# Kernel optimization log

Hardware: AMD Instinct MI355X
Metric: run time of the kernel (lower is better)

## Reference

```python
import jax, jax.numpy as jnp
import numpy as np

B, Z, A = 1024, 512, 8          # batch_size, z_dim, action_dim
AH, ZH = 64, 512                # action_hidden_dim, z_hidden_dim
N_NEG = 100                     # n_neg_actions
TEMP = 0.1                      # temperature
TOP_K = (1, 3, 10)


def forward_model(z, a, Wa, ba, W1, b1, W2, b2):
    # MLP forward model with skip connection (z_delta=True):
    # embed action, concat with z, 2-layer MLP predicting a delta.
    h_a = jax.nn.relu(a @ Wa + ba)                                   # [..., AH]
    h = jax.nn.relu(jnp.concatenate([jnp.broadcast_to(z, a.shape[:-1] + (Z,)), h_a], axis=-1) @ W1 + b1)  # [..., ZH]
    delta = h @ W2 + b2                                              # [..., Z]
    return z + delta


def setup_inputs() -> dict:
    key = jax.random.key(0)
    ks = jax.random.split(key, 8)
    def w(k, shape, fan_in):
        return jax.random.normal(k, shape, jnp.float32) / np.float32(np.sqrt(fan_in))
    z = jax.random.normal(ks[0], (B, Z), jnp.float32)
    z_next = jax.random.normal(ks[1], (B, Z), jnp.float32)
    z_next_hat = jax.random.normal(ks[2], (B, Z), jnp.float32)
    actions = jax.random.normal(ks[3], (B, A), jnp.float32)
    Wa = w(ks[4], (A, AH), A)
    ba = jnp.zeros((AH,), jnp.float32)
    W1 = w(ks[5], (Z + AH, ZH), Z + AH)
    b1 = jnp.zeros((ZH,), jnp.float32)
    W2 = w(ks[6], (ZH, Z), ZH)
    b2 = jnp.zeros((Z,), jnp.float32)
    return {"z": z, "z_next": z_next, "z_next_hat": z_next_hat, "actions": actions,
            "Wa": Wa, "ba": ba, "W1": W1, "b1": b1, "W2": W2, "b2": b2}


def reference(z, z_next, z_next_hat, actions, Wa, ba, W1, b1, W2, b2):
    # ControlCPC.compute_loss with dot_product_similarity, vectorized:
    # the Python loop over n_neg_actions rolled-action forward-model calls
    # becomes one batched [n-1, B, ...] forward-model evaluation.
    batch = z.shape[0]
    n = min(N_NEG, batch)
    sim = z_next @ z_next_hat.T                                      # [B, B] positives on diagonal
    shifts = jnp.arange(1, n)
    neg_actions = jax.vmap(lambda i: jnp.roll(actions, -i, axis=0))(shifts)  # [n-1, B, A]
    z_hat_neg = forward_model(z[None], neg_actions, Wa, ba, W1, b1, W2, b2)  # [n-1, B, Z]
    neg_sim = jnp.einsum('nbz,bz->bn', z_hat_neg, z_next)            # diag of similarity per shift
    sim_mat = jnp.concatenate([sim, neg_sim], axis=1)                # [B, B+n-1]
    # INCE loss, positives on diagonal
    logp = jax.nn.log_softmax(sim_mat / jnp.float32(TEMP), axis=1)
    loss = -jnp.mean(jnp.diagonal(logp))                             # diagonal takes first B entries
    labels = jnp.arange(batch)[:, None]
    accs = []
    for k in TOP_K:
        _, preds = jax.lax.top_k(sim_mat, k)                         # [B, k]
        accs.append(jnp.mean((preds == labels).astype(jnp.float32)) * k)
    return (loss, accs[0], accs[1], accs[2])
```

## Files before the change

### kernel.cpp

```cpp
#include <hip/hip_runtime.h>
#include <math.h>

#define B_SZ 1024
#define Z_DIM 512
#define A_DIM 8
#define AH 64
#define ZH 512
#define NNEG 99
#define INV_T 10.0f

typedef __attribute__((ext_vector_type(8))) short short8;
typedef __attribute__((ext_vector_type(4))) float f32x4;

__device__ __forceinline__ void cvt8(float4 x0, float4 x1, short8& hi, short8& lo) {
    float xs[8] = {x0.x, x0.y, x0.z, x0.w, x1.x, x1.y, x1.z, x1.w};
#pragma unroll
    for (int i = 0; i < 8; ++i) {
        unsigned uu = __float_as_uint(xs[i]);
        hi[i] = (short)(uu >> 16);
        float hf = __uint_as_float(uu & 0xffff0000u);
        lo[i] = (short)(__float_as_uint(xs[i] - hf) >> 16);
    }
}
__device__ __forceinline__ void cvt8s(const float* xs, short8& hi, short8& lo) {
#pragma unroll
    for (int i = 0; i < 8; ++i) {
        unsigned uu = __float_as_uint(xs[i]);
        hi[i] = (short)(uu >> 16);
        float hf = __uint_as_float(uu & 0xffff0000u);
        lo[i] = (short)(__float_as_uint(xs[i] - hf) >> 16);
    }
}

__device__ __forceinline__ int sw(int m, int kb) { return m * 8 + (kb ^ (m & 7)); }

struct MfmaSmem {
    short Ah[4096]; short Al[4096];
    union {
        struct { short Bh[4096]; short Bl[4096]; } t;
        float Bn[64][68];
    } b;
};
struct Seg3Smem {
    float LA[32][68]; float LB[32][68];
    float sact[64][A_DIM]; float sWa[A_DIM * AH]; float sba[AH];
};

__global__ __launch_bounds__(256) void fused_gemm(
    const float* __restrict__ z, const float* __restrict__ z_next,
    const float* __restrict__ z_next_hat, const float* __restrict__ actions,
    const float* __restrict__ Wa, const float* __restrict__ ba,
    const float* __restrict__ W1, const float* __restrict__ b1,
    const float* __restrict__ W2,
    float* __restrict__ sim, float* __restrict__ u, float* __restrict__ v,
    float* __restrict__ g, unsigned* __restrict__ cnt)
{
    __shared__ union { MfmaSmem m; Seg3Smem s; } sm;

    const int id = blockIdx.x;
    const int tid = threadIdx.x;
    if (id == 0 && tid == 0) atomicExch(cnt, 0u);

    if (id >= 512) {
        int t = id - 512;
        int bn0 = (t & 7) * 64, bm0 = (t >> 3) * 64;
        const float* W1h = W1 + Z_DIM * ZH;
        for (int i = tid; i < 64 * A_DIM; i += 256)
            (&sm.s.sact[0][0])[i] = actions[bm0 * A_DIM + i];
        for (int i = tid; i < A_DIM * AH; i += 256) sm.s.sWa[i] = Wa[i];
        if (tid < AH) sm.s.sba[tid] = ba[tid];
        __syncthreads();
        int tm = (tid >> 4) << 2, tn = (tid & 15) << 2;
        float acc[4][4] = {};
        for (int k0 = 0; k0 < 64; k0 += 32) {
#pragma unroll
            for (int i = 0; i < 8; ++i) {
                int lin = tid + i * 256;
                int c = lin & 31, r = lin >> 5;
                int kc = k0 + c;
                float val = sm.s.sba[kc];
#pragma unroll
                for (int k = 0; k < A_DIM; ++k) val += sm.s.sact[r][k] * sm.s.sWa[k * AH + kc];
                sm.s.LA[c][r] = fmaxf(val, 0.0f);
            }
#pragma unroll
            for (int i = 0; i < 2; ++i) {
                int f = tid + i * 256;
                int r = f >> 4, c = (f & 15) * 4;
                *(float4*)&sm.s.LB[r][c] = *(const float4*)&W1h[(k0 + r) * ZH + bn0 + c];
            }
            __syncthreads();
#pragma unroll
            for (int k = 0; k < 32; ++k) {
                float4 a4 = *(const float4*)&sm.s.LA[k][tm];
                float4 b4 = *(const float4*)&sm.s.LB[k][tn];
                float a[4] = {a4.x, a4.y, a4.z, a4.w};
                float b[4] = {b4.x, b4.y, b4.z, b4.w};
#pragma unroll
                for (int i = 0; i < 4; ++i)
#pragma unroll
                    for (int j = 0; j < 4; ++j) acc[i][j] += a[i] * b[j];
            }
            __syncthreads();
        }
#pragma unroll
        for (int i = 0; i < 4; ++i) {
            float4 o = {acc[i][0], acc[i][1], acc[i][2], acc[i][3]};
            *(float4*)&g[(bm0 + tm + i) * ZH + bn0 + tn] = o;
        }
        return;
    }

    const float* Aop; const float* Bop; const float* bias = nullptr;
    float* C; int N; bool btrans; int bm0, bn0;
    if (id < 256) {
        int t = id; bn0 = (t & 15) * 64; bm0 = (t >> 4) * 64;
        Aop = z_next; Bop = z_next_hat; C = sim; N = 1024; btrans = true;
    } else if (id < 384) {
        int t = id - 256; bn0 = (t & 7) * 64; bm0 = (t >> 3) * 64;
        Aop = z; Bop = W1; C = u; N = 512; btrans = false; bias = b1;
    } else {
        int t = id - 384; bn0 = (t & 7) * 64; bm0 = (t >> 3) * 64;
        Aop = z_next; Bop = W2; C = v; N = 512; btrans = true;
    }

    const int lane = tid & 63, wv = tid >> 6;
    const int lm = lane & 15, lq = lane >> 4;
    const int wm = (wv >> 1) * 32, wn = (wv & 1) * 32;
    const int sr = tid >> 2, sq = tid & 3;
    short8* Ah8 = (short8*)sm.m.Ah; short8* Al8 = (short8*)sm.m.Al;
    short8* Bh8 = (short8*)sm.m.b.t.Bh; short8* Bl8 = (short8*)sm.m.b.t.Bl;
    f32x4 acc[2][2] = {};

    for (int k0 = 0; k0 < 512; k0 += 64) {
        {
            const float* base = &Aop[(bm0 + sr) * 512 + k0 + sq * 16];
            float4 x0 = *(const float4*)(base + 0), x1 = *(const float4*)(base + 4);
            float4 x2 = *(const float4*)(base + 8), x3 = *(const float4*)(base + 12);
            short8 h, l;
            cvt8(x0, x1, h, l); Ah8[sw(sr, 2 * sq)] = h;     Al8[sw(sr, 2 * sq)] = l;
            cvt8(x2, x3, h, l); Ah8[sw(sr, 2 * sq + 1)] = h; Al8[sw(sr, 2 * sq + 1)] = l;
        }
        if (btrans) {
            const float* base = &Bop[(bn0 + sr) * 512 + k0 + sq * 16];
            float4 x0 = *(const float4*)(base + 0), x1 = *(const float4*)(base + 4);
            float4 x2 = *(const float4*)(base + 8), x3 = *(const float4*)(base + 12);
            short8 h, l;
            cvt8(x0, x1, h, l); Bh8[sw(sr, 2 * sq)] = h;     Bl8[sw(sr, 2 * sq)] = l;
            cvt8(x2, x3, h, l); Bh8[sw(sr, 2 * sq + 1)] = h; Bl8[sw(sr, 2 * sq + 1)] = l;
        } else {
#pragma unroll
            for (int i = 0; i < 4; ++i) {
                int f = tid + i * 256;
                int kr = f >> 4, c4 = (f & 15) << 2;
                *(float4*)&sm.m.b.Bn[kr][c4] = *(const float4*)&Bop[(k0 + kr) * 512 + bn0 + c4];
            }
        }
        __syncthreads();
#pragma unroll
        for (int kk = 0; kk < 64; kk += 32) {
            int kbi = (kk >> 3) + lq;
            short8 ah[2], al[2], bh[2], bl[2];
#pragma unroll
            for (int i = 0; i < 2; ++i) {
                ah[i] = Ah8[sw(wm + i * 16 + lm, kbi)];
                al[i] = Al8[sw(wm + i * 16 + lm, kbi)];
            }
            if (btrans) {
#pragma unroll
                for (int j = 0; j < 2; ++j) {
                    bh[j] = Bh8[sw(wn + j * 16 + lm, kbi)];
                    bl[j] = Bl8[sw(wn + j * 16 + lm, kbi)];
                }
            } else {
                int kbase = kk + lq * 8;
#pragma unroll
                for (int j = 0; j < 2; ++j) {
                    int n = wn + j * 16 + lm;
                    float xv[8];
#pragma unroll
                    for (int jj = 0; jj < 8; ++jj) xv[jj] = sm.m.b.Bn[kbase + jj][n];
                    cvt8s(xv, bh[j], bl[j]);
                }
            }
#pragma unroll
            for (int i = 0; i < 2; ++i)
#pragma unroll
                for (int j = 0; j < 2; ++j) {
                    acc[i][j] = __builtin_amdgcn_mfma_f32_16x16x32_bf16(ah[i], bh[j], acc[i][j], 0, 0, 0);
                    acc[i][j] = __builtin_amdgcn_mfma_f32_16x16x32_bf16(ah[i], bl[j], acc[i][j], 0, 0, 0);
                    acc[i][j] = __builtin_amdgcn_mfma_f32_16x16x32_bf16(al[i], bh[j], acc[i][j], 0, 0, 0);
                }
        }
        __syncthreads();
    }
#pragma unroll
    for (int i = 0; i < 2; ++i)
#pragma unroll
        for (int j = 0; j < 2; ++j) {
            int n = bn0 + wn + j * 16 + lm;
            float bb = bias ? bias[n] : 0.0f;
#pragma unroll
            for (int r = 0; r < 4; ++r) {
                int m = bm0 + wm + i * 16 + lq * 4 + r;
                C[m * N + n] = acc[i][j][r] + bb;
            }
        }
}

__global__ __launch_bounds__(256) void row2_kernel(
    const float* __restrict__ sim, const float* __restrict__ u,
    const float* __restrict__ v, const float* __restrict__ g,
    const float* __restrict__ z, const float* __restrict__ z_next,
    const float* __restrict__ b2,
    float* __restrict__ pw, unsigned* __restrict__ cnt, float* __restrict__ out)
{
    const int blk = blockIdx.x;
    const int tid = threadIdx.x;
    const int w = tid >> 6, lane = tid & 63;
    const int b = blk * 4 + w;
    __shared__ float gbuf[8][512];
    __shared__ float rn[4][100];
    __shared__ float sacc[4][4];
    __shared__ float red[256];
    __shared__ int sdone;

    float4 ua = *(const float4*)&u[b * 512 + lane * 4];
    float4 ub = *(const float4*)&u[b * 512 + 256 + lane * 4];
    float4 va = *(const float4*)&v[b * 512 + lane * 4];
    float4 vb = *(const float4*)&v[b * 512 + 256 + lane * 4];

    float p;
    {
        float4 za = *(const float4*)&z[b * 512 + lane * 4];
        float4 zb = *(const float4*)&z[b * 512 + 256 + lane * 4];
        float4 na = *(const float4*)&z_next[b * 512 + lane * 4];
        float4 nb = *(const float4*)&z_next[b * 512 + 256 + lane * 4];
        float4 ca = *(const float4*)&b2[lane * 4];
        float4 cb = *(const float4*)&b2[256 + lane * 4];
        p  = (za.x + ca.x) * na.x + (za.y + ca.y) * na.y + (za.z + ca.z) * na.z + (za.w + ca.w) * na.w;
        p += (zb.x + cb.x) * nb.x + (zb.y + cb.y) * nb.y + (zb.z + cb.z) * nb.z + (zb.w + cb.w) * nb.w;
    }
    for (int off = 32; off; off >>= 1) p += __shfl_down(p, off);
    float c0 = __shfl(p, 0);

    const int J0 = blk * 4;
    for (int it = 0; it < 13; ++it) {
#pragma unroll
        for (int ph = 0; ph < 4; ++ph) {
            int f4i = tid + ph * 256;
            int row = f4i >> 7, c = f4i & 127;
            int idx = it * 8 + row;
            if (idx < 102) {
                int jr = (J0 + 1 + idx) & (B_SZ - 1);
                *(float4*)&gbuf[row][c * 4] = *(const float4*)&g[jr * 512 + c * 4];
            }
        }
        __syncthreads();
        float d[8];
#pragma unroll
        for (int ri = 0; ri < 8; ++ri) {
            float4 g0 = *(const float4*)&gbuf[ri][lane * 4];
            float4 g1 = *(const float4*)&gbuf[ri][256 + lane * 4];
            float t = 0.0f;
            t += fmaxf(ua.x + g0.x, 0.0f) * va.x;
            t += fmaxf(ua.y + g0.y, 0.0f) * va.y;
            t += fmaxf(ua.z + g0.z, 0.0f) * va.z;
            t += fmaxf(ua.w + g0.w, 0.0f) * va.w;
            t += fmaxf(ub.x + g1.x, 0.0f) * vb.x;
            t += fmaxf(ub.y + g1.y, 0.0f) * vb.y;
            t += fmaxf(ub.z + g1.z, 0.0f) * vb.z;
            t += fmaxf(ub.w + g1.w, 0.0f) * vb.w;
            d[ri] = t;
        }
        for (int off = 32; off; off >>= 1) {
#pragma unroll
            for (int ri = 0; ri < 8; ++ri) d[ri] += __shfl_down(d[ri], off);
        }
        if (lane == 0) {
#pragma unroll
            for (int ri = 0; ri < 8; ++ri) {
                int idx = it * 8 + ri;
                int s1 = idx - w;
                if (idx < 102 && s1 >= 0 && s1 < 99) rn[w][s1] = c0 + d[ri];
            }
        }
        __syncthreads();
    }

    float4 sv[4];
#pragma unroll
    for (int i = 0; i < 4; ++i)
        sv[i] = *(const float4*)&sim[b * 1024 + lane * 16 + i * 4];
    float nva = rn[w][lane];
    float nvb = (lane < 35) ? rn[w][lane + 64] : -3.4e38f;
    float diag = sim[b * 1024 + b];

    float m = fmaxf(nva, nvb);
#pragma unroll
    for (int i = 0; i < 4; ++i)
        m = fmaxf(m, fmaxf(fmaxf(sv[i].x, sv[i].y), fmaxf(sv[i].z, sv[i].w)));
    for (int off = 32; off; off >>= 1) m = fmaxf(m, __shfl_xor(m, off));

    float es = 0.0f; int ck = 0;
#pragma unroll
    for (int i = 0; i < 4; ++i) {
        float xs[4] = {sv[i].x, sv[i].y, sv[i].z, sv[i].w};
#pragma unroll
        for (int c = 0; c < 4; ++c) {
            int j = lane * 16 + i * 4 + c;
            float x = xs[c];
            es += __expf((x - m) * INV_T);
            if (x > diag) ck++;
            else if (j < b && x == diag) ck++;
        }
    }
    es += __expf((nva - m) * INV_T);
    if (nva > diag) ck++;
    if (lane < 35) {
        es += __expf((nvb - m) * INV_T);
        if (nvb > diag) ck++;
    }
    for (int off = 32; off; off >>= 1) {
        es += __shfl_down(es, off);
        ck += __shfl_down(ck, off);
    }
    if (lane == 0) {
        float loss_b = (m - diag) * INV_T + logf(es);
        sacc[w][0] = loss_b;
        sacc[w][1] = (ck < 1) ? 1.0f : 0.0f;
        sacc[w][2] = (ck < 3) ? 1.0f : 0.0f;
        sacc[w][3] = (ck < 10) ? 1.0f : 0.0f;
    }
    __syncthreads();
    if (tid == 0) {
#pragma unroll
        for (int c = 0; c < 4; ++c)
            pw[blk * 4 + c] = sacc[0][c] + sacc[1][c] + sacc[2][c] + sacc[3][c];
        __threadfence();
        unsigned old = atomicAdd(cnt, 1u);
        sdone = (old == 255u) ? 1 : 0;
    }
    __syncthreads();
    if (sdone) {
        __threadfence();
        int c = tid & 3;
        float s = 0.0f;
        for (int r = tid >> 2; r < 256; r += 64) s += pw[r * 4 + c];
        red[tid] = s;
        __syncthreads();
        if (tid < 4) {
            float t = 0.0f;
            for (int q = 0; q < 64; ++q) t += red[tid + q * 4];
            out[tid] = t * (1.0f / (float)B_SZ);
        }
    }
}

extern "C" void kernel_launch(void* const* d_in, const int* in_sizes, int n_in,
                              void* d_out, int out_size, void* d_ws, size_t ws_size,
                              hipStream_t stream) {
    const float* z          = (const float*)d_in[0];
    const float* z_next     = (const float*)d_in[1];
    const float* z_next_hat = (const float*)d_in[2];
    const float* actions    = (const float*)d_in[3];
    const float* Wa         = (const float*)d_in[4];
    const float* ba         = (const float*)d_in[5];
    const float* W1         = (const float*)d_in[6];
    const float* b1         = (const float*)d_in[7];
    const float* W2         = (const float*)d_in[8];
    const float* b2         = (const float*)d_in[9];
    float* out = (float*)d_out;

    float* ws  = (float*)d_ws;
    float* sim = ws;
    float* u   = sim + B_SZ * B_SZ;
    float* v   = u + B_SZ * ZH;
    float* g   = v + B_SZ * ZH;
    float* pw  = g + B_SZ * ZH;
    unsigned* cnt = (unsigned*)(pw + 256 * 4);

    fused_gemm<<<640, 256, 0, stream>>>(z, z_next, z_next_hat, actions, Wa, ba,
                                        W1, b1, W2, sim, u, v, g, cnt);
    row2_kernel<<<256, 256, 0, stream>>>(sim, u, v, g, z, z_next, b2, pw, cnt, out);
}
```

Baseline: 135.1 us.

## Pre-transpose W1 and precompute action embedding in a prep kernel

Adds a small prep kernel that transposes W1 into a K-contiguous workspace buffer and computes the ReLU action embedding ha. The main GEMM kernel then uses one uniform transposed-B MFMA path for all four segments, including the action-embedding product, which was previously a scalar FP32 path. This removes the strided shared-memory gathers and per-iteration conversion of the non-transposed W1 operand. The cost is an extra kernel launch, extra workspace traffic, and a serial dependency before the main GEMM.

```diff
diff --git a/kernel.cpp b/kernel.cpp
--- a/kernel.cpp
+++ b/kernel.cpp
@@ -22,139 +22,118 @@
         lo[i] = (short)(__float_as_uint(xs[i] - hf) >> 16);
     }
 }
-__device__ __forceinline__ void cvt8s(const float* xs, short8& hi, short8& lo) {
-#pragma unroll
-    for (int i = 0; i < 8; ++i) {
-        unsigned uu = __float_as_uint(xs[i]);
-        hi[i] = (short)(uu >> 16);
-        float hf = __uint_as_float(uu & 0xffff0000u);
-        lo[i] = (short)(__float_as_uint(xs[i] - hf) >> 16);
-    }
-}
 
 __device__ __forceinline__ int sw(int m, int kb) { return m * 8 + (kb ^ (m & 7)); }
 
-struct MfmaSmem {
-    short Ah[4096]; short Al[4096];
-    union {
-        struct { short Bh[4096]; short Bl[4096]; } t;
-        float Bn[64][68];
-    } b;
-};
-struct Seg3Smem {
-    float LA[32][68]; float LB[32][68];
-    float sact[64][A_DIM]; float sWa[A_DIM * AH]; float sba[AH];
-};
-
-__global__ __launch_bounds__(256) void fused_gemm(
+__global__ __launch_bounds__(256) void prep_kernel(
+    const float* __restrict__ W1, const float* __restrict__ actions,
+    const float* __restrict__ Wa, const float* __restrict__ ba,
+    float* __restrict__ W1T, float* __restrict__ ha, unsigned* __restrict__ cnt)
+{
+    const int id = blockIdx.x, tid = threadIdx.x;
+    if (id == 0 && tid == 0) atomicExch(cnt, 0u);
+    if (id < 72) {
+        __shared__ float L[64][68];
+        int kt = id >> 3, nt = id & 7;
+#pragma unroll
+        for (int i = 0; i < 4; ++i) {
+            int f = tid + i * 256;
+            int r = f >> 4, c4 = (f & 15) << 2;
+            *(float4*)&L[r][c4] = *(const float4*)&W1[(kt * 64 + r) * 512 + nt * 64 + c4];
+        }
+        __syncthreads();
+#pragma unroll
+        for (int i = 0; i < 4; ++i) {
+            int f = tid + i * 256;
+            int r = f >> 4, c4 = (f & 15) << 2;
+            float4 o = {L[c4][r], L[c4 + 1][r], L[c4 + 2][r], L[c4 + 3][r]};
+            *(float4*)&W1T[(nt * 64 + r) * 576 + kt * 64 + c4] = o;
+        }
+    } else if (id < 88) {
+        __shared__ float sWa[A_DIM * 64];
+        __shared__ float sba[64];
+        __shared__ float sact[64][A_DIM];
+        int j0 = (id - 72) * 64;
+        for (int i = tid; i < A_DIM * 64; i += 256) sWa[i] = Wa[i];
+        if (tid < 64) sba[tid] = ba[tid];
+        for (int i = tid; i < 64 * A_DIM; i += 256) (&sact[0][0])[i] = actions[j0 * A_DIM + i];
+        __syncthreads();
+        int r = tid >> 2, c0 = (tid & 3) * 16;
+        float o[16];
+#pragma unroll
+        for (int c = 0; c < 16; ++c) o[c] = sba[c0 + c];
+#pragma unroll
+        for (int k = 0; k < A_DIM; ++k) {
+            float a = sact[r][k];
+#pragma unroll
+            for (int c = 0; c < 16; ++c) o[c] += a * sWa[k * 64 + c0 + c];
+        }
+#pragma unroll
+        for (int c = 0; c < 16; c += 4) {
+            float4 v4 = {fmaxf(o[c], 0.f), fmaxf(o[c + 1], 0.f),
+                         fmaxf(o[c + 2], 0.f), fmaxf(o[c + 3], 0.f)};
+            *(float4*)&ha[(j0 + r) * 64 + c0 + c] = v4;
+        }
+    }
+}
+
+__global__ __launch_bounds__(256) void mm_kernel(
     const float* __restrict__ z, const float* __restrict__ z_next,
-    const float* __restrict__ z_next_hat, const float* __restrict__ actions,
-    const float* __restrict__ Wa, const float* __restrict__ ba,
-    const float* __restrict__ W1, const float* __restrict__ b1,
-    const float* __restrict__ W2,
+    const float* __restrict__ z_next_hat, const float* __restrict__ W1T,
+    const float* __restrict__ b1, const float* __restrict__ W2,
+    const float* __restrict__ ha,
     float* __restrict__ sim, float* __restrict__ u, float* __restrict__ v,
-    float* __restrict__ g, unsigned* __restrict__ cnt)
+    float* __restrict__ g)
 {
-    __shared__ union { MfmaSmem m; Seg3Smem s; } sm;
+    __shared__ short Ah[4096], Al[4096], Bh[4096], Bl[4096];
 
     const int id = blockIdx.x;
     const int tid = threadIdx.x;
-    if (id == 0 && tid == 0) atomicExch(cnt, 0u);
-
-    if (id >= 512) {
-        int t = id - 512;
-        int bn0 = (t & 7) * 64, bm0 = (t >> 3) * 64;
-        const float* W1h = W1 + Z_DIM * ZH;
-        for (int i = tid; i < 64 * A_DIM; i += 256)
-            (&sm.s.sact[0][0])[i] = actions[bm0 * A_DIM + i];
-        for (int i = tid; i < A_DIM * AH; i += 256) sm.s.sWa[i] = Wa[i];
-        if (tid < AH) sm.s.sba[tid] = ba[tid];
-        __syncthreads();
-        int tm = (tid >> 4) << 2, tn = (tid & 15) << 2;
-        float acc[4][4] = {};
-        for (int k0 = 0; k0 < 64; k0 += 32) {
-#pragma unroll
-            for (int i = 0; i < 8; ++i) {
-                int lin = tid + i * 256;
-                int c = lin & 31, r = lin >> 5;
-                int kc = k0 + c;
-                float val = sm.s.sba[kc];
-#pragma unroll
-                for (int k = 0; k < A_DIM; ++k) val += sm.s.sact[r][k] * sm.s.sWa[k * AH + kc];
-                sm.s.LA[c][r] = fmaxf(val, 0.0f);
-            }
-#pragma unroll
-            for (int i = 0; i < 2; ++i) {
-                int f = tid + i * 256;
-                int r = f >> 4, c = (f & 15) * 4;
-                *(float4*)&sm.s.LB[r][c] = *(const float4*)&W1h[(k0 + r) * ZH + bn0 + c];
-            }
-            __syncthreads();
-#pragma unroll
-            for (int k = 0; k < 32; ++k) {
-                float4 a4 = *(const float4*)&sm.s.LA[k][tm];
-                float4 b4 = *(const float4*)&sm.s.LB[k][tn];
-                float a[4] = {a4.x, a4.y, a4.z, a4.w};
-                float b[4] = {b4.x, b4.y, b4.z, b4.w};
-#pragma unroll
-                for (int i = 0; i < 4; ++i)
-#pragma unroll
-                    for (int j = 0; j < 4; ++j) acc[i][j] += a[i] * b[j];
-            }
-            __syncthreads();
-        }
-#pragma unroll
-        for (int i = 0; i < 4; ++i) {
-            float4 o = {acc[i][0], acc[i][1], acc[i][2], acc[i][3]};
-            *(float4*)&g[(bm0 + tm + i) * ZH + bn0 + tn] = o;
-        }
-        return;
-    }
 
     const float* Aop; const float* Bop; const float* bias = nullptr;
-    float* C; int N; bool btrans; int bm0, bn0;
+    float* C; int N, K, lda, ldb, bm0, bn0;
     if (id < 256) {
         int t = id; bn0 = (t & 15) * 64; bm0 = (t >> 4) * 64;
-        Aop = z_next; Bop = z_next_hat; C = sim; N = 1024; btrans = true;
+        Aop = z_next; lda = 512; Bop = z_next_hat; ldb = 512;
+        C = sim; N = 1024; K = 512;
     } else if (id < 384) {
         int t = id - 256; bn0 = (t & 7) * 64; bm0 = (t >> 3) * 64;
-        Aop = z; Bop = W1; C = u; N = 512; btrans = false; bias = b1;
+        Aop = z; lda = 512; Bop = W1T; ldb = 576;
+        C = u; N = 512; K = 512; bias = b1;
+    } else if (id < 512) {
+        int t = id - 384; bn0 = (t & 7) * 64; bm0 = (t >> 3) * 64;
+        Aop = z_next; lda = 512; Bop = W2; ldb = 512;
+        C = v; N = 512; K = 512;
     } else {
-        int t = id - 384; bn0 = (t & 7) * 64; bm0 = (t >> 3) * 64;
-        Aop = z_next; Bop = W2; C = v; N = 512; btrans = true;
+        int t = id - 512; bn0 = (t & 7) * 64; bm0 = (t >> 3) * 64;
+        Aop = ha; lda = 64; Bop = W1T + 512; ldb = 576;
+        C = g; N = 512; K = 64;
     }
 
     const int lane = tid & 63, wv = tid >> 6;
     const int lm = lane & 15, lq = lane >> 4;
     const int wm = (wv >> 1) * 32, wn = (wv & 1) * 32;
     const int sr = tid >> 2, sq = tid & 3;
-    short8* Ah8 = (short8*)sm.m.Ah; short8* Al8 = (short8*)sm.m.Al;
-    short8* Bh8 = (short8*)sm.m.b.t.Bh; short8* Bl8 = (short8*)sm.m.b.t.Bl;
+    short8* Ah8 = (short8*)Ah; short8* Al8 = (short8*)Al;
+    short8* Bh8 = (short8*)Bh; short8* Bl8 = (short8*)Bl;
     f32x4 acc[2][2] = {};
 
-    for (int k0 = 0; k0 < 512; k0 += 64) {
+    for (int k0 = 0; k0 < K; k0 += 64) {
         {
-            const float* base = &Aop[(bm0 + sr) * 512 + k0 + sq * 16];
+            const float* base = &Aop[(bm0 + sr) * lda + k0 + sq * 16];
             float4 x0 = *(const float4*)(base + 0), x1 = *(const float4*)(base + 4);
             float4 x2 = *(const float4*)(base + 8), x3 = *(const float4*)(base + 12);
             short8 h, l;
             cvt8(x0, x1, h, l); Ah8[sw(sr, 2 * sq)] = h;     Al8[sw(sr, 2 * sq)] = l;
             cvt8(x2, x3, h, l); Ah8[sw(sr, 2 * sq + 1)] = h; Al8[sw(sr, 2 * sq + 1)] = l;
         }
-        if (btrans) {
-            const float* base = &Bop[(bn0 + sr) * 512 + k0 + sq * 16];
+        {
+            const float* base = &Bop[(bn0 + sr) * ldb + k0 + sq * 16];
             float4 x0 = *(const float4*)(base + 0), x1 = *(const float4*)(base + 4);
             float4 x2 = *(const float4*)(base + 8), x3 = *(const float4*)(base + 12);
             short8 h, l;
             cvt8(x0, x1, h, l); Bh8[sw(sr, 2 * sq)] = h;     Bl8[sw(sr, 2 * sq)] = l;
             cvt8(x2, x3, h, l); Bh8[sw(sr, 2 * sq + 1)] = h; Bl8[sw(sr, 2 * sq + 1)] = l;
-        } else {
-#pragma unroll
-            for (int i = 0; i < 4; ++i) {
-                int f = tid + i * 256;
-                int kr = f >> 4, c4 = (f & 15) << 2;
-                *(float4*)&sm.m.b.Bn[kr][c4] = *(const float4*)&Bop[(k0 + kr) * 512 + bn0 + c4];
-            }
         }
         __syncthreads();
 #pragma unroll
@@ -165,23 +144,8 @@
             for (int i = 0; i < 2; ++i) {
                 ah[i] = Ah8[sw(wm + i * 16 + lm, kbi)];
                 al[i] = Al8[sw(wm + i * 16 + lm, kbi)];
-            }
-            if (btrans) {
-#pragma unroll
-                for (int j = 0; j < 2; ++j) {
-                    bh[j] = Bh8[sw(wn + j * 16 + lm, kbi)];
-                    bl[j] = Bl8[sw(wn + j * 16 + lm, kbi)];
-                }
-            } else {
-                int kbase = kk + lq * 8;
-#pragma unroll
-                for (int j = 0; j < 2; ++j) {
-                    int n = wn + j * 16 + lm;
-                    float xv[8];
-#pragma unroll
-                    for (int jj = 0; jj < 8; ++jj) xv[jj] = sm.m.b.Bn[kbase + jj][n];
-                    cvt8s(xv, bh[j], bl[j]);
-                }
+                bh[i] = Bh8[sw(wn + i * 16 + lm, kbi)];
+                bl[i] = Bl8[sw(wn + i * 16 + lm, kbi)];
             }
 #pragma unroll
             for (int i = 0; i < 2; ++i)
@@ -372,15 +336,18 @@
     const float* b2         = (const float*)d_in[9];
     float* out = (float*)d_out;
 
-    float* ws  = (float*)d_ws;
-    float* sim = ws;
-    float* u   = sim + B_SZ * B_SZ;
-    float* v   = u + B_SZ * ZH;
-    float* g   = v + B_SZ * ZH;
-    float* pw  = g + B_SZ * ZH;
+    float* ws   = (float*)d_ws;
+    float* sim  = ws;
+    float* u    = sim + B_SZ * B_SZ;
+    float* v    = u + B_SZ * ZH;
+    float* g    = v + B_SZ * ZH;
+    float* W1T  = g + B_SZ * ZH;
+    float* ha   = W1T + 512 * 576;
+    float* pw   = ha + B_SZ * AH;
     unsigned* cnt = (unsigned*)(pw + 256 * 4);
 
-    fused_gemm<<<640, 256, 0, stream>>>(z, z_next, z_next_hat, actions, Wa, ba,
-                                        W1, b1, W2, sim, u, v, g, cnt);
+    prep_kernel<<<88, 256, 0, stream>>>(W1, actions, Wa, ba, W1T, ha, cnt);
+    mm_kernel<<<640, 256, 0, stream>>>(z, z_next, z_next_hat, W1T, b1, W2, ha,
+                                       sim, u, v, g);
     row2_kernel<<<256, 256, 0, stream>>>(sim, u, v, g, z, z_next, b2, pw, cnt, out);
 }
```

After: 124.1 us. 1.09x faster.
